# Optimization experiments

Measured on AMD Instinct MI355X. Metric: run time of the kernel, lower is better.

The kernel has to match this reference:

```python
import jax, jax.numpy as jnp
import numpy as np
from jax import lax

K_TOP = 16        # self.k
TEMP = 5.0        # temperature at step 0 (tempIncr=5; external temperatureUpdate schedule, see notes)
EPS = 1e-20


def setup_inputs() -> dict:
    key = jax.random.key(0)
    k1, k2 = jax.random.split(key)
    logits = jax.random.normal(k1, (64, 1024), dtype=jnp.float32)          # (N, D)
    u = jax.random.uniform(k2, (32, 64, 1024), dtype=jnp.float32)          # (BS, N, D)
    gn = -jnp.log(-jnp.log(u + EPS) + EPS)                                 # Gumbel noise
    return {"logits": logits, "gn": gn}


def reference(logits, gn):
    # logits: (N, D); gn: (BS, N, D)
    D = logits.shape[-1]
    perturbed = logits[None, :, :] + gn                                    # (BS, N, D)
    # double top-k: top_k values' indices, then top_k over indices sorts them descending
    _, idx = lax.top_k(perturbed, K_TOP)                                   # (BS, N, k)
    idx_desc, _ = lax.top_k(idx, K_TOP)                                    # indices sorted descending
    topk = idx_desc[..., ::-1]                                             # ascending, (BS, N, k)
    hard = jax.nn.one_hot(topk, D, dtype=logits.dtype)                     # (BS, N, k, D)
    # exclusive cumsum over the k axis
    cum_mask = jnp.cumsum(hard, axis=-2) - hard                            # (BS, N, k, D)
    prob_exp = jnp.exp(logits)[None, :, None, :]                           # broadcast of tiled (BS, N, k, D)
    scores = (jnp.log(prob_exp * (1.0 - cum_mask + EPS)) + gn[:, :, None, :]) / TEMP
    soft = jax.nn.softmax(scores, axis=-1)                                 # (BS, N, k, D)
    return lax.stop_gradient(hard - soft) + soft
```

## Files before the change

### kernel.cpp

```cpp
#include <hip/hip_runtime.h>
#include <math.h>

#define K_TOP 16
#define D_DIM 1024

__global__ __launch_bounds__(256) void dps_topk_kernel(
    const float* __restrict__ logits,
    const float* __restrict__ gn,
    float* __restrict__ out)
{
    const int q    = blockIdx.x;
    const int r    = q & 63;
    const int tid  = threadIdx.x;
    const int lane = tid & 63;
    const int wave = tid >> 6;

    __shared__ int sel_lds[K_TOP];

    if (wave == 0) {
        float v[16];
        const float* lrow = logits + (size_t)r * D_DIM;
        const float* grow = gn + (size_t)q * D_DIM;
        #pragma unroll
        for (int j = 0; j < 16; ++j) {
            const int d = lane + 64 * j;
            v[j] = lrow[d] + grow[d];
        }

        unsigned chosen = 0;
        int my_sel = 0;

        for (int round = 0; round < K_TOP; ++round) {
            float bv = -INFINITY;
            int   bi = 0x7fffffff;
            #pragma unroll
            for (int j = 0; j < 16; ++j) {
                if (!(chosen & (1u << j))) {
                    if (v[j] > bv) { bv = v[j]; bi = lane + 64 * j; }
                }
            }
            #pragma unroll
            for (int off = 32; off > 0; off >>= 1) {
                const float ov = __shfl_xor(bv, off);
                const int   oi = __shfl_xor(bi, off);
                if (ov > bv || (ov == bv && oi < bi)) { bv = ov; bi = oi; }
            }
            if (lane == (bi & 63)) chosen |= 1u << (bi >> 6);
            if (lane == round)     my_sel = bi;
        }

        int rank = 0;
        #pragma unroll
        for (int j = 0; j < K_TOP; ++j) {
            const int other = __shfl(my_sel, j);
            rank += (other < my_sel) ? 1 : 0;
        }
        if (lane < K_TOP) sel_lds[rank] = my_sel;
    }
    __syncthreads();

    float* orow = out + (size_t)q * (K_TOP * D_DIM);
    const int d0 = tid * 4;
    #pragma unroll
    for (int k = 0; k < K_TOP; ++k) {
        const int s = sel_lds[k];
        float4 val;
        val.x = (d0 + 0 == s) ? 1.0f : 0.0f;
        val.y = (d0 + 1 == s) ? 1.0f : 0.0f;
        val.z = (d0 + 2 == s) ? 1.0f : 0.0f;
        val.w = (d0 + 3 == s) ? 1.0f : 0.0f;
        *reinterpret_cast<float4*>(orow + (size_t)k * D_DIM + d0) = val;
    }
}

extern "C" void kernel_launch(void* const* d_in, const int* in_sizes, int n_in,
                              void* d_out, int out_size, void* d_ws, size_t ws_size,
                              hipStream_t stream) {
    const float* logits = (const float*)d_in[0];
    const float* gn     = (const float*)d_in[1];
    float* out          = (float*)d_out;

    dps_topk_kernel<<<dim3(2048), dim3(256), 0, stream>>>(logits, gn, out);
}
```

Before: 36.89 us.

## Process four rows per block, one wave each, with vectorized loads and nontemporal stores

Each of the four waves in a block now runs the top-k selection for its own row, where before only wave 0 worked and the other three waves idled. The grid shrinks accordingly. Each lane loads 16 contiguous elements with float4 loads, so the index mapping becomes lane*16+j. Output writes become nontemporal float4 stores done per wave for its row, so the 64 MB one-hot write bypasses cache. The main cost being removed is the idle-wave imbalance during selection; in exchange each wave now writes a whole row alone, and the tie-breaking order is preserved through the global-index comparison.

```diff
diff --git a/kernel.cpp b/kernel.cpp
--- a/kernel.cpp
+++ b/kernel.cpp
@@ -3,73 +3,88 @@
 
 #define K_TOP 16
 #define D_DIM 1024
+#define ROWS_PER_BLOCK 4
+
+typedef float f32x4 __attribute__((ext_vector_type(4)));
 
 __global__ __launch_bounds__(256) void dps_topk_kernel(
     const float* __restrict__ logits,
     const float* __restrict__ gn,
     float* __restrict__ out)
 {
-    const int q    = blockIdx.x;
-    const int r    = q & 63;
     const int tid  = threadIdx.x;
     const int lane = tid & 63;
     const int wave = tid >> 6;
+    const int q    = blockIdx.x * ROWS_PER_BLOCK + wave;
+    const int r    = q & 63;
 
-    __shared__ int sel_lds[K_TOP];
+    __shared__ int sel_lds[ROWS_PER_BLOCK][K_TOP];
 
-    if (wave == 0) {
-        float v[16];
-        const float* lrow = logits + (size_t)r * D_DIM;
-        const float* grow = gn + (size_t)q * D_DIM;
+    float v[16];
+    {
+        const f32x4* l4 = reinterpret_cast<const f32x4*>(
+            logits + (size_t)r * D_DIM + lane * 16);
+        const f32x4* g4 = reinterpret_cast<const f32x4*>(
+            gn + (size_t)q * D_DIM + lane * 16);
+        #pragma unroll
+        for (int c = 0; c < 4; ++c) {
+            const f32x4 a = l4[c];
+            const f32x4 b = g4[c];
+            v[c * 4 + 0] = a.x + b.x;
+            v[c * 4 + 1] = a.y + b.y;
+            v[c * 4 + 2] = a.z + b.z;
+            v[c * 4 + 3] = a.w + b.w;
+        }
+    }
+
+    unsigned chosen = 0;
+    int my_sel = 0;
+    for (int round = 0; round < K_TOP; ++round) {
+        float bv = -INFINITY;
+        int   bi = 0x7fffffff;
         #pragma unroll
         for (int j = 0; j < 16; ++j) {
-            const int d = lane + 64 * j;
-            v[j] = lrow[d] + grow[d];
+            if (!(chosen & (1u << j))) {
+                if (v[j] > bv) { bv = v[j]; bi = lane * 16 + j; }
+            }
         }
+        #pragma unroll
+        for (int off = 32; off > 0; off >>= 1) {
+            const float ov = __shfl_xor(bv, off);
+            const int   oi = __shfl_xor(bi, off);
+            if (ov > bv || (ov == bv && oi < bi)) { bv = ov; bi = oi; }
+        }
+        if (lane == (bi >> 4)) chosen |= 1u << (bi & 15);
+        if (lane == round)     my_sel = bi;
+    }
 
-        unsigned chosen = 0;
-        int my_sel = 0;
-
-        for (int round = 0; round < K_TOP; ++round) {
-            float bv = -INFINITY;
-            int   bi = 0x7fffffff;
-            #pragma unroll
-            for (int j = 0; j < 16; ++j) {
-                if (!(chosen & (1u << j))) {
-                    if (v[j] > bv) { bv = v[j]; bi = lane + 64 * j; }
-                }
-            }
-            #pragma unroll
-            for (int off = 32; off > 0; off >>= 1) {
-                const float ov = __shfl_xor(bv, off);
-                const int   oi = __shfl_xor(bi, off);
-                if (ov > bv || (ov == bv && oi < bi)) { bv = ov; bi = oi; }
-            }
-            if (lane == (bi & 63)) chosen |= 1u << (bi >> 6);
-            if (lane == round)     my_sel = bi;
-        }
-
-        int rank = 0;
-        #pragma unroll
-        for (int j = 0; j < K_TOP; ++j) {
-            const int other = __shfl(my_sel, j);
-            rank += (other < my_sel) ? 1 : 0;
-        }
-        if (lane < K_TOP) sel_lds[rank] = my_sel;
+    int rank = 0;
+    #pragma unroll
+    for (int j = 0; j < K_TOP; ++j) {
+        const int other = __shfl(my_sel, j);
+        rank += (other < my_sel) ? 1 : 0;
     }
+    if (lane < K_TOP) sel_lds[wave][rank] = my_sel;
     __syncthreads();
 
     float* orow = out + (size_t)q * (K_TOP * D_DIM);
-    const int d0 = tid * 4;
     #pragma unroll
     for (int k = 0; k < K_TOP; ++k) {
-        const int s = sel_lds[k];
-        float4 val;
-        val.x = (d0 + 0 == s) ? 1.0f : 0.0f;
-        val.y = (d0 + 1 == s) ? 1.0f : 0.0f;
-        val.z = (d0 + 2 == s) ? 1.0f : 0.0f;
-        val.w = (d0 + 3 == s) ? 1.0f : 0.0f;
-        *reinterpret_cast<float4*>(orow + (size_t)k * D_DIM + d0) = val;
+        const int s  = sel_lds[wave][k];
+        const int sv = s >> 2;
+        f32x4 hot;
+        hot.x = ((s & 3) == 0) ? 1.0f : 0.0f;
+        hot.y = ((s & 3) == 1) ? 1.0f : 0.0f;
+        hot.z = ((s & 3) == 2) ? 1.0f : 0.0f;
+        hot.w = ((s & 3) == 3) ? 1.0f : 0.0f;
+        const f32x4 zero = {0.f, 0.f, 0.f, 0.f};
+        f32x4* krow = reinterpret_cast<f32x4*>(orow + k * D_DIM);
+        #pragma unroll
+        for (int c = 0; c < 4; ++c) {
+            const int f4idx = c * 64 + lane;
+            const f32x4 val = (f4idx == sv) ? hot : zero;
+            __builtin_nontemporal_store(val, krow + f4idx);
+        }
     }
 }
 
@@ -80,5 +95,6 @@
     const float* gn     = (const float*)d_in[1];
     float* out          = (float*)d_out;
 
-    dps_topk_kernel<<<dim3(2048), dim3(256), 0, stream>>>(logits, gn, out);
+    dps_topk_kernel<<<dim3(2048 / ROWS_PER_BLOCK), dim3(256), 0, stream>>>(
+        logits, gn, out);
 }
```

After: 41.99 us. 13.8% more time.
